# Kernel tuning notes

Measured on AMD Instinct MI355X. Metric: run time of the kernel, lower is better.

Reference implementation:

```python
import jax, jax.numpy as jnp
import numpy as np

B, H, W, C = 8, 128, 128, 384
WS, SHIFT, NH = 8, 4, 12
N = WS * WS            # tokens per window = 64
HD = C // NH           # head dim = 32
SCALE = HD ** -0.5


def _rel_pos_index():
    ch, cw = np.meshgrid(np.arange(WS), np.arange(WS), indexing='ij')
    cf = np.stack([ch.ravel(), cw.ravel()])            # (2, N)
    rel = cf[:, :, None] - cf[:, None, :]              # (2, N, N)
    rel = rel.transpose(1, 2, 0)                       # (N, N, 2)
    rel[:, :, 0] += WS - 1
    rel[:, :, 1] += WS - 1
    rel[:, :, 0] *= 2 * WS - 1
    return jnp.asarray(rel.sum(-1))                    # (N, N) int

REL_IDX = _rel_pos_index()


def _shift_mask():
    # standard Swin SW-MSA mask, built once with numpy
    img = np.zeros((1, H, W, 1), np.float32)
    cnt = 0
    for hs in (slice(0, -WS), slice(-WS, -SHIFT), slice(-SHIFT, None)):
        for ws_ in (slice(0, -WS), slice(-WS, -SHIFT), slice(-SHIFT, None)):
            img[:, hs, ws_, :] = cnt
            cnt += 1
    m = img.reshape(1, H // WS, WS, W // WS, WS, 1).transpose(0, 1, 3, 2, 4, 5)
    m = m.reshape(-1, N)                               # (nW, N)
    am = m[:, None, :] - m[:, :, None]                 # (nW, N, N)
    return np.where(am != 0, np.float32(-100.0), np.float32(0.0))


def _ln(x, g, b, eps=1e-5):
    mu = x.mean(-1, keepdims=True)
    var = ((x - mu) ** 2).mean(-1, keepdims=True)
    return (x - mu) * jax.lax.rsqrt(var + eps) * g + b


def setup_inputs() -> dict:
    key = jax.random.key(0)
    ks = jax.random.split(key, 10)
    s = 0.02
    return {
        'x': jax.random.normal(ks[0], (B, H * W, C), jnp.float32),
        'qkv_w': jax.random.normal(ks[1], (3 * C, C), jnp.float32) * s,
        'qkv_b': jnp.zeros((3 * C,), jnp.float32),
        'proj_w': jax.random.normal(ks[2], (C, C), jnp.float32) * s,
        'proj_b': jnp.zeros((C,), jnp.float32),
        'rel_bias_table': jax.random.normal(ks[3], ((2 * WS - 1) ** 2, NH), jnp.float32) * s,
        'g1': jnp.ones((C,), jnp.float32), 'b1': jnp.zeros((C,), jnp.float32),
        'g2': jnp.ones((C,), jnp.float32), 'b2': jnp.zeros((C,), jnp.float32),
        'fc1_w': jax.random.normal(ks[4], (4 * C, C), jnp.float32) * s,
        'fc1_b': jnp.zeros((4 * C,), jnp.float32),
        'fc2_w': jax.random.normal(ks[5], (C, 4 * C), jnp.float32) * s,
        'fc2_b': jnp.zeros((C,), jnp.float32),
        'attn_mask': jnp.asarray(_shift_mask()),       # (nW, N, N)
    }


def reference(x, qkv_w, qkv_b, proj_w, proj_b, rel_bias_table, g1, b1, g2, b2,
              fc1_w, fc1_b, fc2_w, fc2_b, attn_mask):
    shortcut = x
    h = _ln(x, g1, b1).reshape(B, H, W, C)
    # cyclic shift (SW-MSA)
    h = jnp.roll(h, (-SHIFT, -SHIFT), axis=(1, 2))
    # window partition -> (B*nW, N, C)
    nWh, nWw = H // WS, W // WS
    hw = h.reshape(B, nWh, WS, nWw, WS, C).transpose(0, 1, 3, 2, 4, 5)
    hw = hw.reshape(B * nWh * nWw, N, C)
    # qkv projection
    qkv = jnp.einsum('bnc,dc->bnd', hw, qkv_w) + qkv_b   # (Bw, N, 3C)
    qkv = qkv.reshape(-1, N, 3, NH, HD).transpose(2, 0, 3, 1, 4)
    q, k, v = qkv[0], qkv[1], qkv[2]                    # (Bw, NH, N, HD)
    attn = jnp.einsum('bhnd,bhmd->bhnm', q * SCALE, k)  # (Bw, NH, N, N)
    bias = rel_bias_table[REL_IDX.reshape(-1)].reshape(N, N, NH)
    attn = attn + bias.transpose(2, 0, 1)[None]
    # shift mask: attn viewed as (B, nW, NH, N, N) + mask (nW, 1, N, N)
    nW = nWh * nWw
    attn = attn.reshape(B, nW, NH, N, N) + attn_mask[None, :, None]
    attn = jax.nn.softmax(attn.reshape(-1, NH, N, N), axis=-1)
    out = jnp.einsum('bhnm,bhmd->bnhd', attn, v).reshape(-1, N, C)
    out = jnp.einsum('bnc,dc->bnd', out, proj_w) + proj_b
    # window reverse + un-shift
    out = out.reshape(B, nWh, nWw, WS, WS, C).transpose(0, 1, 3, 2, 4, 5)
    out = out.reshape(B, H, W, C)
    out = jnp.roll(out, (SHIFT, SHIFT), axis=(1, 2)).reshape(B, H * W, C)
    x = shortcut + out
    # MLP block
    h2 = _ln(x, g2, b2)
    h2 = jax.nn.gelu(jnp.einsum('blc,dc->bld', h2, fc1_w) + fc1_b, approximate=False)
    h2 = jnp.einsum('bld,cd->blc', h2, fc2_w) + fc2_b
    return x + h2
```

## Files before the change

### kernel.cpp

```cpp
#include <hip/hip_runtime.h>
#include <hip/hip_bf16.h>
#include <math.h>

typedef __attribute__((ext_vector_type(4))) float f32x4;
typedef __attribute__((ext_vector_type(8))) short bf16x8;

__device__ __forceinline__ unsigned short f2bf(float f) {
  unsigned int x = __builtin_bit_cast(unsigned int, f);
  x += 0x7fffu + ((x >> 16) & 1u);
  return (unsigned short)(x >> 16);
}

__device__ __forceinline__ void gload_lds16(const void* g, void* l) {
  __builtin_amdgcn_global_load_lds(
      (const __attribute__((address_space(1))) unsigned int*)g,
      (__attribute__((address_space(3))) unsigned int*)l, 16, 0, 0);
}

__global__ void cvt_f32_bf16(const float* __restrict__ s, unsigned short* __restrict__ d, int n) {
  int i = blockIdx.x * 256 + threadIdx.x;
  if (i < n) d[i] = f2bf(s[i]);
}

template <int REMAP>
__global__ __launch_bounds__(256)
void ln_kernel(const float* __restrict__ x, const float* __restrict__ g,
               const float* __restrict__ b, unsigned short* __restrict__ dst_o) {
  int r = blockIdx.x * 4 + (threadIdx.x >> 6);
  int lane = threadIdx.x & 63;
  size_t src;
  if (REMAP) {
    int w = r >> 6, t = r & 63;
    int bb = w >> 8, wi = (w >> 4) & 15, wj = w & 15;
    int i = t >> 3, j = t & 7;
    int p = (wi * 8 + i + 4) & 127, q = (wj * 8 + j + 4) & 127;
    src = ((size_t)bb * 16384 + p * 128 + q) * 384;
  } else {
    src = (size_t)r * 384;
  }
  float v[6];
  float s = 0.f, s2 = 0.f;
#pragma unroll
  for (int m = 0; m < 6; ++m) {
    v[m] = x[src + lane + 64 * m];
    s += v[m];
    s2 += v[m] * v[m];
  }
#pragma unroll
  for (int o2 = 1; o2 < 64; o2 <<= 1) {
    s += __shfl_xor(s, o2);
    s2 += __shfl_xor(s2, o2);
  }
  float mu = s * (1.f / 384.f);
  float var = s2 * (1.f / 384.f) - mu * mu;
  float ri = rsqrtf(var + 1e-5f);
  size_t dst = (size_t)r * 384;
#pragma unroll
  for (int m = 0; m < 6; ++m) {
    int c = lane + 64 * m;
    dst_o[dst + c] = f2bf((v[m] - mu) * ri * g[c] + b[c]);
  }
}

template <int EPI>
__global__ __launch_bounds__(256, 2)
void gemm_bt(const unsigned short* __restrict__ A, const unsigned short* __restrict__ Bw,
             const float* __restrict__ bias, int M, int N, int K, int NT,
             unsigned short* __restrict__ Obf, const float* __restrict__ resid,
             float* __restrict__ Of) {
  __shared__ unsigned short smA[2][128 * 64];
  __shared__ unsigned short smB[2][128 * 64];
  const int tid = threadIdx.x;
  const int lane = tid & 63;
  const int wid = tid >> 6;
  const int wm = wid >> 1, wn = wid & 1;
  const int li = lane & 15, lg = lane >> 4;

  const int nwg = gridDim.x;
  const int orig = blockIdx.x;
  const int q = nwg >> 3, r = nwg & 7;
  const int xcd = orig & 7, loc = orig >> 3;
  const int wg = (xcd < r ? xcd * (q + 1) : r * (q + 1) + (xcd - r) * q) + loc;
  const int m0 = (wg / NT) * 128;
  const int n0 = (wg % NT) * 128;

  const int srow = wid * 32 + (lane >> 3);
  const int scol = ((lane & 7) ^ (lane >> 3)) * 8;
  const unsigned short* gA = A + (size_t)(m0 + srow) * K + scol;
  const unsigned short* gB = Bw + (size_t)(n0 + srow) * K + scol;

  f32x4 acc[4][4] = {};
  const int nk = K >> 6;

  const int fswz = (li & 7) << 3;

#pragma unroll
  for (int c = 0; c < 4; ++c) {
    gload_lds16(gA + (size_t)(c * 8) * K, &smA[0][(wid * 32 + c * 8) * 64]);
    gload_lds16(gB + (size_t)(c * 8) * K, &smB[0][(wid * 32 + c * 8) * 64]);
  }
  __syncthreads();

  for (int k0 = 0; k0 < nk; ++k0) {
    const int cur = k0 & 1;
    if (k0 + 1 < nk) {
#pragma unroll
      for (int c = 0; c < 4; ++c) {
        gload_lds16(gA + (size_t)(c * 8) * K + (k0 + 1) * 64,
                    &smA[cur ^ 1][(wid * 32 + c * 8) * 64]);
        gload_lds16(gB + (size_t)(c * 8) * K + (k0 + 1) * 64,
                    &smB[cur ^ 1][(wid * 32 + c * 8) * 64]);
      }
    }
#pragma unroll
    for (int kk = 0; kk < 2; ++kk) {
      bf16x8 a[4], bb[4];
#pragma unroll
      for (int f = 0; f < 4; ++f) {
        a[f] = *(const bf16x8*)&smA[cur][(wm * 64 + f * 16 + li) * 64 + ((kk * 32 + lg * 8) ^ fswz)];
        bb[f] = *(const bf16x8*)&smB[cur][(wn * 64 + f * 16 + li) * 64 + ((kk * 32 + lg * 8) ^ fswz)];
      }
#pragma unroll
      for (int mf = 0; mf < 4; ++mf)
#pragma unroll
        for (int nf = 0; nf < 4; ++nf)
          acc[mf][nf] = __builtin_amdgcn_mfma_f32_16x16x32_bf16(a[mf], bb[nf], acc[mf][nf], 0, 0, 0);
    }
    __syncthreads();
  }

#pragma unroll
  for (int mf = 0; mf < 4; ++mf) {
#pragma unroll
    for (int r2 = 0; r2 < 4; ++r2) {
      int mrow = m0 + wm * 64 + mf * 16 + lg * 4 + r2;
      size_t orow = (size_t)mrow;
      if (EPI == 2) {
        int w = mrow >> 6, t = mrow & 63;
        int bb2 = w >> 8, wi = (w >> 4) & 15, wj = w & 15;
        int i = t >> 3, j = t & 7;
        int p = (wi * 8 + i + 4) & 127, qq = (wj * 8 + j + 4) & 127;
        orow = (size_t)bb2 * 16384 + p * 128 + qq;
      }
#pragma unroll
      for (int nf = 0; nf < 4; ++nf) {
        int col = n0 + wn * 64 + nf * 16 + li;
        float v = acc[mf][nf][r2] + bias[col];
        if (EPI == 0) {
          Obf[(size_t)mrow * N + col] = f2bf(v);
        } else if (EPI == 1) {
          float y = 1.5957691f * (v + 0.044715f * v * v * v);
          float gl = v / (1.f + __expf(-y));
          Obf[(size_t)mrow * N + col] = f2bf(gl);
        } else if (EPI == 2) {
          Of[orow * 384 + col] = v + resid[orow * 384 + col];
        } else {
          Of[(size_t)mrow * N + col] = v + resid[(size_t)mrow * N + col];
        }
      }
    }
  }
}

__global__ __launch_bounds__(256, 2)
void attn_kernel(const unsigned short* __restrict__ qkv, const float* __restrict__ btab,
                 const float* __restrict__ mask, unsigned short* __restrict__ out) {
  __shared__ unsigned short v_lds[4][64 * 40];
  __shared__ unsigned short p_lds[4][64 * 72];
  const int w = blockIdx.x;
  const int tid = threadIdx.x;
  const int wid = tid >> 6, lane = tid & 63;
  const int li = lane & 15, lg = lane >> 4;
  const float* mrow = mask + (size_t)(w & 255) * 4096;
  const size_t base = (size_t)w * 64;
  const float SC = 0.17677669529663688f;

#pragma unroll 1
  for (int hi = 0; hi < 3; ++hi) {
    int h = wid * 3 + hi;
    bf16x8 aq[4], bk[4];
#pragma unroll
    for (int f = 0; f < 4; ++f) {
      size_t off = (base + f * 16 + li) * 1152 + h * 32 + lg * 8;
      aq[f] = *(const bf16x8*)&qkv[off];
      bk[f] = *(const bf16x8*)&qkv[off + 384];
    }
    f32x4 s[4][4] = {};
#pragma unroll
    for (int mf = 0; mf < 4; ++mf)
#pragma unroll
      for (int nf = 0; nf < 4; ++nf)
        s[mf][nf] = __builtin_amdgcn_mfma_f32_16x16x32_bf16(aq[mf], bk[nf], s[mf][nf], 0, 0, 0);

    {
      const unsigned short* vp = &qkv[(base + lane) * 1152 + 768 + h * 32];
      unsigned short* dp = &v_lds[wid][lane * 40];
#pragma unroll
      for (int c = 0; c < 4; ++c) *(bf16x8*)&dp[c * 8] = *(const bf16x8*)&vp[c * 8];
    }

#pragma unroll
    for (int mf = 0; mf < 4; ++mf) {
#pragma unroll
      for (int r = 0; r < 4; ++r) {
        int m = mf * 16 + lg * 4 + r;
        float mx = -1e30f;
#pragma unroll
        for (int nf = 0; nf < 4; ++nf) {
          int n = nf * 16 + li;
          int ridx = ((m >> 3) - (n >> 3) + 7) * 15 + (m & 7) - (n & 7) + 7;
          float val = s[mf][nf][r] * SC + btab[ridx * 12 + h] + mrow[m * 64 + n];
          s[mf][nf][r] = val;
          mx = fmaxf(mx, val);
        }
#pragma unroll
        for (int o2 = 1; o2 < 16; o2 <<= 1) mx = fmaxf(mx, __shfl_xor(mx, o2));
        float sum = 0.f;
#pragma unroll
        for (int nf = 0; nf < 4; ++nf) {
          float e = __expf(s[mf][nf][r] - mx);
          s[mf][nf][r] = e;
          sum += e;
        }
#pragma unroll
        for (int o2 = 1; o2 < 16; o2 <<= 1) sum += __shfl_xor(sum, o2);
        float inv = 1.f / sum;
#pragma unroll
        for (int nf = 0; nf < 4; ++nf) s[mf][nf][r] *= inv;
      }
    }

#pragma unroll
    for (int mf = 0; mf < 4; ++mf)
#pragma unroll
      for (int nf = 0; nf < 4; ++nf)
#pragma unroll
        for (int r = 0; r < 4; ++r) {
          int m = mf * 16 + lg * 4 + r, n = nf * 16 + li;
          p_lds[wid][m * 72 + n] = f2bf(s[mf][nf][r]);
        }

    f32x4 o[4][2] = {};
#pragma unroll
    for (int kf = 0; kf < 2; ++kf) {
      bf16x8 bv[2];
#pragma unroll
      for (int df = 0; df < 2; ++df) {
        bf16x8 t;
#pragma unroll
        for (int e = 0; e < 8; ++e)
          t[e] = (short)v_lds[wid][(kf * 32 + lg * 8 + e) * 40 + df * 16 + li];
        bv[df] = t;
      }
#pragma unroll
      for (int mf = 0; mf < 4; ++mf) {
        bf16x8 pa = *(const bf16x8*)&p_lds[wid][(mf * 16 + li) * 72 + kf * 32 + lg * 8];
#pragma unroll
        for (int df = 0; df < 2; ++df)
          o[mf][df] = __builtin_amdgcn_mfma_f32_16x16x32_bf16(pa, bv[df], o[mf][df], 0, 0, 0);
      }
    }

#pragma unroll
    for (int mf = 0; mf < 4; ++mf)
#pragma unroll
      for (int df = 0; df < 2; ++df)
#pragma unroll
        for (int r = 0; r < 4; ++r) {
          size_t row = base + mf * 16 + lg * 4 + r;
          out[row * 384 + h * 32 + df * 16 + li] = f2bf(o[mf][df][r]);
        }
  }
}

extern "C" void kernel_launch(void* const* d_in, const int* in_sizes, int n_in,
                              void* d_out, int out_size, void* d_ws, size_t ws_size,
                              hipStream_t stream) {
  const float* x      = (const float*)d_in[0];
  const float* qkv_w  = (const float*)d_in[1];
  const float* qkv_b  = (const float*)d_in[2];
  const float* proj_w = (const float*)d_in[3];
  const float* proj_b = (const float*)d_in[4];
  const float* rel    = (const float*)d_in[5];
  const float* g1     = (const float*)d_in[6];
  const float* b1     = (const float*)d_in[7];
  const float* g2     = (const float*)d_in[8];
  const float* b2     = (const float*)d_in[9];
  const float* fc1_w  = (const float*)d_in[10];
  const float* fc1_b  = (const float*)d_in[11];
  const float* fc2_w  = (const float*)d_in[12];
  const float* fc2_b  = (const float*)d_in[13];
  const float* mask   = (const float*)d_in[14];
  float* out = (float*)d_out;
  char* ws = (char*)d_ws;

  const int M = 131072;
  unsigned short* hw     = (unsigned short*)ws;
  unsigned short* qkv    = (unsigned short*)(ws + 100663296);
  unsigned short* hmid   = (unsigned short*)ws;
  unsigned short* attn_o = (unsigned short*)(ws + 402653184);
  unsigned short* ln2o   = attn_o;
  float*          x1     = (float*)(ws + 503316480);
  unsigned short* wq     = (unsigned short*)(ws + 704643072);
  unsigned short* wp     = wq + 442368;
  unsigned short* w1     = wp + 147456;
  unsigned short* w2     = w1 + 589824;

  cvt_f32_bf16<<<(442368 + 255) / 256, 256, 0, stream>>>(qkv_w, wq, 442368);
  cvt_f32_bf16<<<(147456 + 255) / 256, 256, 0, stream>>>(proj_w, wp, 147456);
  cvt_f32_bf16<<<(589824 + 255) / 256, 256, 0, stream>>>(fc1_w, w1, 589824);
  cvt_f32_bf16<<<(589824 + 255) / 256, 256, 0, stream>>>(fc2_w, w2, 589824);

  ln_kernel<1><<<M / 4, 256, 0, stream>>>(x, g1, b1, hw);

  gemm_bt<0><<<9 * 1024, 256, 0, stream>>>(hw, wq, qkv_b, M, 1152, 384, 9, qkv, nullptr, nullptr);

  attn_kernel<<<2048, 256, 0, stream>>>(qkv, rel, mask, attn_o);

  gemm_bt<2><<<3 * 1024, 256, 0, stream>>>(attn_o, wp, proj_b, M, 384, 384, 3, nullptr, x, x1);

  ln_kernel<0><<<M / 4, 256, 0, stream>>>(x1, g2, b2, ln2o);

  gemm_bt<1><<<12 * 1024, 256, 0, stream>>>(ln2o, w1, fc1_b, M, 1536, 384, 12, hmid, nullptr, nullptr);

  gemm_bt<3><<<3 * 1024, 256, 0, stream>>>(hmid, w2, fc2_b, M, 384, 1536, 3, nullptr, x1, out);
}
```

Before: 1.241 ms.

## Use 8-wave GEMM blocks and store mid residual x1 in bf16

GEMM workgroups grow from 4 to 8 waves, each computing a 64x32 sub-tile, so register pressure per wave drops and more waves are available to hide latency. Separately, the intermediate residual x1 is now stored as bf16 instead of fp32. A new bf16-input LayerNorm reads it, and the final GEMM adds it back from bf16. This halves the traffic for that intermediate but lowers the precision of the residual path, which could affect accuracy.

```diff
diff --git a/kernel.cpp b/kernel.cpp
--- a/kernel.cpp
+++ b/kernel.cpp
@@ -9,6 +9,10 @@
   unsigned int x = __builtin_bit_cast(unsigned int, f);
   x += 0x7fffu + ((x >> 16) & 1u);
   return (unsigned short)(x >> 16);
+}
+__device__ __forceinline__ float bf2f(unsigned short u) {
+  unsigned int x = ((unsigned int)u) << 16;
+  return __builtin_bit_cast(float, x);
 }
 
 __device__ __forceinline__ void gload_lds16(const void* g, void* l) {
@@ -62,18 +66,51 @@
   }
 }
 
+__global__ __launch_bounds__(256)
+void ln_bf16(const unsigned short* __restrict__ x, const float* __restrict__ g,
+             const float* __restrict__ b, unsigned short* __restrict__ dst_o) {
+  int r = blockIdx.x * 4 + (threadIdx.x >> 6);
+  int lane = threadIdx.x & 63;
+  size_t src = (size_t)r * 384;
+  float v[6];
+  float s = 0.f, s2 = 0.f;
+#pragma unroll
+  for (int m = 0; m < 3; ++m) {
+    unsigned int u = *(const unsigned int*)&x[src + lane * 2 + 128 * m];
+    v[2 * m] = bf2f((unsigned short)(u & 0xffffu));
+    v[2 * m + 1] = bf2f((unsigned short)(u >> 16));
+    s += v[2 * m] + v[2 * m + 1];
+    s2 += v[2 * m] * v[2 * m] + v[2 * m + 1] * v[2 * m + 1];
+  }
+#pragma unroll
+  for (int o2 = 1; o2 < 64; o2 <<= 1) {
+    s += __shfl_xor(s, o2);
+    s2 += __shfl_xor(s2, o2);
+  }
+  float mu = s * (1.f / 384.f);
+  float var = s2 * (1.f / 384.f) - mu * mu;
+  float ri = rsqrtf(var + 1e-5f);
+#pragma unroll
+  for (int m = 0; m < 3; ++m) {
+    int c = lane * 2 + 128 * m;
+    unsigned int lo = f2bf((v[2 * m] - mu) * ri * g[c] + b[c]);
+    unsigned int hi = f2bf((v[2 * m + 1] - mu) * ri * g[c + 1] + b[c + 1]);
+    *(unsigned int*)&dst_o[src + c] = lo | (hi << 16);
+  }
+}
+
 template <int EPI>
-__global__ __launch_bounds__(256, 2)
+__global__ __launch_bounds__(512, 2)
 void gemm_bt(const unsigned short* __restrict__ A, const unsigned short* __restrict__ Bw,
              const float* __restrict__ bias, int M, int N, int K, int NT,
-             unsigned short* __restrict__ Obf, const float* __restrict__ resid,
+             unsigned short* __restrict__ Obf, const void* __restrict__ resid,
              float* __restrict__ Of) {
   __shared__ unsigned short smA[2][128 * 64];
   __shared__ unsigned short smB[2][128 * 64];
   const int tid = threadIdx.x;
   const int lane = tid & 63;
   const int wid = tid >> 6;
-  const int wm = wid >> 1, wn = wid & 1;
+  const int wm = wid >> 2, wn = wid & 3;
   const int li = lane & 15, lg = lane >> 4;
 
   const int nwg = gridDim.x;
@@ -84,20 +121,19 @@
   const int m0 = (wg / NT) * 128;
   const int n0 = (wg % NT) * 128;
 
-  const int srow = wid * 32 + (lane >> 3);
+  const int srow = wid * 8 + (lane >> 3);
   const int scol = ((lane & 7) ^ (lane >> 3)) * 8;
   const unsigned short* gA = A + (size_t)(m0 + srow) * K + scol;
   const unsigned short* gB = Bw + (size_t)(n0 + srow) * K + scol;
 
-  f32x4 acc[4][4] = {};
+  f32x4 acc[4][2] = {};
   const int nk = K >> 6;
-
   const int fswz = (li & 7) << 3;
 
 #pragma unroll
-  for (int c = 0; c < 4; ++c) {
-    gload_lds16(gA + (size_t)(c * 8) * K, &smA[0][(wid * 32 + c * 8) * 64]);
-    gload_lds16(gB + (size_t)(c * 8) * K, &smB[0][(wid * 32 + c * 8) * 64]);
+  for (int c = 0; c < 2; ++c) {
+    gload_lds16(gA + (size_t)(c * 64) * K, &smA[0][c * 4096 + wid * 512]);
+    gload_lds16(gB + (size_t)(c * 64) * K, &smB[0][c * 4096 + wid * 512]);
   }
   __syncthreads();
 
@@ -105,25 +141,26 @@
     const int cur = k0 & 1;
     if (k0 + 1 < nk) {
 #pragma unroll
-      for (int c = 0; c < 4; ++c) {
-        gload_lds16(gA + (size_t)(c * 8) * K + (k0 + 1) * 64,
-                    &smA[cur ^ 1][(wid * 32 + c * 8) * 64]);
-        gload_lds16(gB + (size_t)(c * 8) * K + (k0 + 1) * 64,
-                    &smB[cur ^ 1][(wid * 32 + c * 8) * 64]);
+      for (int c = 0; c < 2; ++c) {
+        gload_lds16(gA + (size_t)(c * 64) * K + (k0 + 1) * 64,
+                    &smA[cur ^ 1][c * 4096 + wid * 512]);
+        gload_lds16(gB + (size_t)(c * 64) * K + (k0 + 1) * 64,
+                    &smB[cur ^ 1][c * 4096 + wid * 512]);
       }
     }
 #pragma unroll
     for (int kk = 0; kk < 2; ++kk) {
-      bf16x8 a[4], bb[4];
-#pragma unroll
-      for (int f = 0; f < 4; ++f) {
+      bf16x8 a[4], bb[2];
+#pragma unroll
+      for (int f = 0; f < 4; ++f)
         a[f] = *(const bf16x8*)&smA[cur][(wm * 64 + f * 16 + li) * 64 + ((kk * 32 + lg * 8) ^ fswz)];
-        bb[f] = *(const bf16x8*)&smB[cur][(wn * 64 + f * 16 + li) * 64 + ((kk * 32 + lg * 8) ^ fswz)];
-      }
+#pragma unroll
+      for (int f = 0; f < 2; ++f)
+        bb[f] = *(const bf16x8*)&smB[cur][(wn * 32 + f * 16 + li) * 64 + ((kk * 32 + lg * 8) ^ fswz)];
 #pragma unroll
       for (int mf = 0; mf < 4; ++mf)
 #pragma unroll
-        for (int nf = 0; nf < 4; ++nf)
+        for (int nf = 0; nf < 2; ++nf)
           acc[mf][nf] = __builtin_amdgcn_mfma_f32_16x16x32_bf16(a[mf], bb[nf], acc[mf][nf], 0, 0, 0);
     }
     __syncthreads();
@@ -143,8 +180,8 @@
         orow = (size_t)bb2 * 16384 + p * 128 + qq;
       }
 #pragma unroll
-      for (int nf = 0; nf < 4; ++nf) {
-        int col = n0 + wn * 64 + nf * 16 + li;
+      for (int nf = 0; nf < 2; ++nf) {
+        int col = n0 + wn * 32 + nf * 16 + li;
         float v = acc[mf][nf][r2] + bias[col];
         if (EPI == 0) {
           Obf[(size_t)mrow * N + col] = f2bf(v);
@@ -153,9 +190,11 @@
           float gl = v / (1.f + __expf(-y));
           Obf[(size_t)mrow * N + col] = f2bf(gl);
         } else if (EPI == 2) {
-          Of[orow * 384 + col] = v + resid[orow * 384 + col];
+          const float* rx = (const float*)resid;
+          Obf[orow * 384 + col] = f2bf(v + rx[orow * 384 + col]);
         } else {
-          Of[(size_t)mrow * N + col] = v + resid[(size_t)mrow * N + col];
+          const unsigned short* rx = (const unsigned short*)resid;
+          Of[(size_t)mrow * N + col] = v + bf2f(rx[(size_t)mrow * N + col]);
         }
       }
     }
@@ -300,8 +339,8 @@
   unsigned short* hmid   = (unsigned short*)ws;
   unsigned short* attn_o = (unsigned short*)(ws + 402653184);
   unsigned short* ln2o   = attn_o;
-  float*          x1     = (float*)(ws + 503316480);
-  unsigned short* wq     = (unsigned short*)(ws + 704643072);
+  unsigned short* x1b    = (unsigned short*)(ws + 503316480);
+  unsigned short* wq     = (unsigned short*)(ws + 603979776);
   unsigned short* wp     = wq + 442368;
   unsigned short* w1     = wp + 147456;
   unsigned short* w2     = w1 + 589824;
@@ -313,15 +352,15 @@
 
   ln_kernel<1><<<M / 4, 256, 0, stream>>>(x, g1, b1, hw);
 
-  gemm_bt<0><<<9 * 1024, 256, 0, stream>>>(hw, wq, qkv_b, M, 1152, 384, 9, qkv, nullptr, nullptr);
+  gemm_bt<0><<<9 * 1024, 512, 0, stream>>>(hw, wq, qkv_b, M, 1152, 384, 9, qkv, nullptr, nullptr);
 
   attn_kernel<<<2048, 256, 0, stream>>>(qkv, rel, mask, attn_o);
 
-  gemm_bt<2><<<3 * 1024, 256, 0, stream>>>(attn_o, wp, proj_b, M, 384, 384, 3, nullptr, x, x1);
-
-  ln_kernel<0><<<M / 4, 256, 0, stream>>>(x1, g2, b2, ln2o);
-
-  gemm_bt<1><<<12 * 1024, 256, 0, stream>>>(ln2o, w1, fc1_b, M, 1536, 384, 12, hmid, nullptr, nullptr);
-
-  gemm_bt<3><<<3 * 1024, 256, 0, stream>>>(hmid, w2, fc2_b, M, 384, 1536, 3, nullptr, x1, out);
-}
+  gemm_bt<2><<<3 * 1024, 512, 0, stream>>>(attn_o, wp, proj_b, M, 384, 384, 3, x1b, x, nullptr);
+
+  ln_bf16<<<M / 4, 256, 0, stream>>>(x1b, g2, b2, ln2o);
+
+  gemm_bt<1><<<12 * 1024, 512, 0, stream>>>(ln2o, w1, fc1_b, M, 1536, 384, 12, hmid, nullptr, nullptr);
+
+  gemm_bt<3><<<3 * 1024, 512, 0, stream>>>(hmid, w2, fc2_b, M, 384, 1536, 3, nullptr, x1b, out);
+}
```

New measurement: 1.233 ms. Within noise of the previous version (-0.6%).
